# Optimization experiments

Measured on AMD Instinct MI355X. Metric: run time of the kernel, lower is better.

The kernel has to match this reference:

```python
import jax, jax.numpy as jnp
import numpy as np

FG_FRACTION = 0.5
FG_THRESH = 0.7
BG_HI = 0.5
BG_LO = 0.1
BATCHSIZE = 256
FG_ROIS = int(round(FG_FRACTION * BATCHSIZE))  # 128


def setup_inputs() -> dict:
    key = jax.random.key(0)
    k1, k2, k3 = jax.random.split(key, 3)
    N, K, C = 80000, 256, 81
    IMG = 800.0

    def make_boxes(k, n):
        ka, kb = jax.random.split(k)
        xy = jax.random.uniform(ka, (1, n, 2), dtype=jnp.float32) * (IMG - 136.0)
        wh = jax.random.uniform(kb, (1, n, 2), dtype=jnp.float32) * 128.0 + 8.0
        return jnp.concatenate([xy, xy + wh], axis=-1)  # valid x1<x2, y1<y2

    proposals = make_boxes(k1, N)          # (1, N, 4)
    gt_boxes = make_boxes(k2, K)           # (1, K, 4)
    cls = jax.random.randint(k3, (K,), 1, C)
    gt_labels = jax.nn.one_hot(cls, C, dtype=jnp.float32)[None]  # (1, K, C)
    return {"proposals": proposals, "gt_labels": gt_labels, "gt_boxes": gt_boxes}


def _iou(a, b):
    # a: (M,4), b: (K,4); keras_rcnn +1-pixel convention
    area_a = (a[:, 2] - a[:, 0] + 1.0) * (a[:, 3] - a[:, 1] + 1.0)
    area_b = (b[:, 2] - b[:, 0] + 1.0) * (b[:, 3] - b[:, 1] + 1.0)
    x1 = jnp.maximum(a[:, None, 0], b[None, :, 0])
    y1 = jnp.maximum(a[:, None, 1], b[None, :, 1])
    x2 = jnp.minimum(a[:, None, 2], b[None, :, 2])
    y2 = jnp.minimum(a[:, None, 3], b[None, :, 3])
    iw = jnp.maximum(x2 - x1 + 1.0, 0.0)
    ih = jnp.maximum(y2 - y1 + 1.0, 0.0)
    inter = iw * ih  # (M, K)
    return inter / (area_a[:, None] + area_b[None, :] - inter)


def _bbox_transform(ex, gt):
    ew = ex[:, 2] - ex[:, 0] + 1.0
    eh = ex[:, 3] - ex[:, 1] + 1.0
    ecx = ex[:, 0] + 0.5 * ew
    ecy = ex[:, 1] + 0.5 * eh
    gw = gt[:, 2] - gt[:, 0] + 1.0
    gh = gt[:, 3] - gt[:, 1] + 1.0
    gcx = gt[:, 0] + 0.5 * gw
    gcy = gt[:, 1] + 0.5 * gh
    return jnp.stack([(gcx - ecx) / ew, (gcy - ecy) / eh,
                      jnp.log(gw / ew), jnp.log(gh / eh)], axis=1)  # (B, 4)


def _forward(proposals, gt_labels, gt_boxes):
    all_rois = jnp.concatenate([proposals[0], gt_boxes[0]], axis=0)  # (M, 4)
    gt_b = gt_boxes[0]    # (K, 4)
    gt_l = gt_labels[0]   # (K, C)
    C = gt_l.shape[1]

    ov = _iou(all_rois, gt_b)               # (M, K)
    gt_assign = jnp.argmax(ov, axis=1)      # (M,)
    max_ov = jnp.max(ov, axis=1)            # (M,)

    fg_mask = max_ov >= FG_THRESH
    bg_mask = (max_ov < BG_HI) & (max_ov >= BG_LO)

    M = all_rois.shape[0]
    order = jnp.arange(M)
    # deterministic stand-in for random shuffle: candidates first, in index order
    fg_sorted = jnp.argsort(jnp.where(fg_mask, order, M + order))
    bg_sorted = jnp.argsort(jnp.where(bg_mask, order, M + order))
    num_fg = jnp.sum(fg_mask.astype(jnp.int32))
    fg_take = jnp.minimum(FG_ROIS, num_fg)

    pos = jnp.arange(BATCHSIZE)
    is_fg_slot = pos < fg_take
    keep = jnp.where(is_fg_slot,
                     fg_sorted[jnp.clip(pos, 0, M - 1)],
                     bg_sorted[jnp.clip(pos - fg_take, 0, M - 1)])  # (B,)

    rois = all_rois[keep]                    # (B, 4)
    labels = gt_l[gt_assign[keep]]           # (B, C)
    # set_label_background: bg slots -> one-hot class 0
    bg_onehot = jax.nn.one_hot(0, C, dtype=labels.dtype)
    labels = jnp.where(is_fg_slot[:, None], labels, bg_onehot[None, :])

    assigned_gt = gt_b[gt_assign[keep]]      # (B, 4)
    targets = _bbox_transform(rois, assigned_gt)  # (B, 4)

    # expand to N x 4K: only the argmax class (if > 0) gets nonzero targets
    clss = jnp.argmax(labels, axis=1)        # (B,)
    cls_oh = jnp.where((clss > 0)[:, None],
                       jax.nn.one_hot(clss, C, dtype=targets.dtype), 0.0)  # (B, C)
    bbox_targets = (cls_oh[:, :, None] * targets[:, None, :]).reshape(BATCHSIZE, 4 * C)

    return rois[None], labels[None], bbox_targets[None]


def reference(proposals, gt_labels, gt_boxes):
    return _forward(proposals, gt_labels, gt_boxes)
```

## Files before the change

kernel.cpp:

```cpp
#include <hip/hip_runtime.h>

#define FG_THRESH 0.7f
#define BG_HI 0.5f
#define BG_LO 0.1f
#define BATCH 256
#define FG_ROIS 128
#define KGT 256
#define CLS 81
#define CPT 5
#define NCHPAD 1280
#define NBIN 26
#define NSPAN 6

typedef unsigned long long ull;

__global__ __launch_bounds__(256) void k_iou(
    const float* __restrict__ proposals,
    const float* __restrict__ gt_boxes,
    int N, int M,
    int* __restrict__ gt_assign,
    ull* __restrict__ fgm,
    ull* __restrict__ bgm)
{
    __shared__ float4 gshE[KGT];
    __shared__ float garea[KGT];
    __shared__ ull pbx[4][NBIN], pby[4][NBIN];
    __shared__ ull intX[4][NBIN][NSPAN], intY[4][NBIN][NSPAN];

    int tid = threadIdx.x;
    int wv = tid >> 6, lane = tid & 63;

    float4 g = ((const float4*)gt_boxes)[tid];
    gshE[tid] = g;
    garea[tid] = (g.z - g.x + 1.0f) * (g.w - g.y + 1.0f);

    for (int b = 0; b < NBIN; ++b) {
        float hiE = 32.0f * (float)(b + 1);
        float loE = 32.0f * (float)b - 1.0f;
        ull mx = __ballot((g.x < hiE) && (g.z > loE));
        ull my = __ballot((g.y < hiE) && (g.w > loE));
        if (lane == 0) { pbx[wv][b] = mx; pby[wv][b] = my; }
    }
    __syncthreads();

    if (tid < 104) {
        int c = tid / NBIN, b = tid % NBIN;
        ull m = pbx[c][b];
        intX[c][b][0] = m;
        #pragma unroll
        for (int s = 1; s < NSPAN; ++s) {
            int bb = b + s;
            if (bb < NBIN) m |= pbx[c][bb];
            intX[c][b][s] = m;
        }
    } else if (tid >= 128 && tid < 232) {
        int u = tid - 128;
        int c = u / NBIN, b = u % NBIN;
        ull m = pby[c][b];
        intY[c][b][0] = m;
        #pragma unroll
        for (int s = 1; s < NSPAN; ++s) {
            int bb = b + s;
            if (bb < NBIN) m |= pby[c][bb];
            intY[c][b][s] = m;
        }
    }
    __syncthreads();

    int c = lane & 3;
    int rj = lane >> 2;

    int ch = blockIdx.x;
    int roi = ch * 64 + wv * 16 + rj;
    bool val = (roi < M);

    float4 a;
    if (val) a = (roi < N) ? ((const float4*)proposals)[roi] : gshE[roi - N];
    else     a = gshE[0];
    float az1 = a.z + 1.0f, aw1 = a.w + 1.0f;
    float area_a = (a.z - a.x + 1.0f) * (a.w - a.y + 1.0f);

    int b1x = (int)(a.x * 0.03125f);
    int b2x = min((int)(az1 * 0.03125f), NBIN - 1);
    int b1y = (int)(a.y * 0.03125f);
    int b2y = min((int)(aw1 * 0.03125f), NBIN - 1);
    int sx = b2x - b1x;
    int sy = b2y - b1y;

    ull mbits = val ? (intX[c][b1x][sx] & intY[c][b1y][sy]) : 0ull;

    float best = 0.0f;
    int bestk = 0;
    while (mbits) {
        int j = __ffsll(mbits) - 1;
        mbits &= mbits - 1;
        int k = (c << 6) + j;
        float4 gg = gshE[k];
        float x1 = fmaxf(a.x, gg.x);
        float y1 = fmaxf(a.y, gg.y);
        float x2 = fminf(a.z, gg.z);
        float y2 = fminf(a.w, gg.w);
        float iw = fmaxf(x2 - x1 + 1.0f, 0.0f);
        float ih = fmaxf(y2 - y1 + 1.0f, 0.0f);
        float inter = iw * ih;
        float q = inter / (area_a + garea[k] - inter);
        if (q > best) { best = q; bestk = k; }
    }

    #pragma unroll
    for (int d = 1; d < 4; d <<= 1) {
        float ob = __shfl_xor(best, d);
        int   kb = __shfl_xor(bestk, d);
        if (ob > best || (ob == best && kb < bestk)) { best = ob; bestk = kb; }
    }
    float bset = __shfl(best, (lane & 15) * 4);
    int   bk   = __shfl(bestk, (lane & 15) * 4);

    int roi2 = ch * 64 + wv * 16 + (lane & 15);
    bool isv = (lane < 16) && (roi2 < M);
    bool fgp = isv && (bset >= FG_THRESH);
    bool bgp = isv && (bset < BG_HI) && (bset >= BG_LO);
    if (isv) gt_assign[roi2] = bk;

    ull mf = __ballot(fgp);
    ull mb = __ballot(bgp);
    if (lane == 0) {
        ((unsigned short*)fgm)[(ch << 2) | wv] = (unsigned short)mf;
        ((unsigned short*)bgm)[(ch << 2) | wv] = (unsigned short)mb;
    }
}

__global__ __launch_bounds__(256) void k_finish(
    const float* __restrict__ proposals,
    const float* __restrict__ gt_boxes,
    const float* __restrict__ gt_labels,
    int N, int NCH,
    const int* __restrict__ gt_assign,
    const ull* __restrict__ fgm,
    const ull* __restrict__ bgm,
    float* __restrict__ out_rois,
    float* __restrict__ out_labels,
    float4* __restrict__ out_bbox)
{
    __shared__ ull sf[NCHPAD], sb[NCHPAD], sn[NCHPAD];
    __shared__ int pf[NCHPAD], pb[NCHPAD], pn[NCHPAD];
    __shared__ int fgl[FG_ROIS], bgl[BATCH], nbl[BATCH];
    __shared__ int wtot[3][4];
    __shared__ int lm_cls[8];
    __shared__ float4 lm_t[8];

    int tid = threadIdx.x;
    int lane = tid & 63, wv = tid >> 6;

    for (int idx = tid; idx < NCHPAD; idx += 256) {
        bool v = (idx < NCH);
        ull fv = v ? fgm[idx] : 0ull;
        ull bv = v ? bgm[idx] : 0ull;
        sf[idx] = fv;
        sb[idx] = bv;
        sn[idx] = v ? ~bv : 0ull;
    }
    __syncthreads();

    int lo = tid * CPT;
    int pc0 = 0, pc1 = 0;
    #pragma unroll
    for (int r = 0; r < CPT; ++r) {
        pc0 += __popcll(sf[lo + r]);
        pc1 += __popcll(sb[lo + r]);
    }
    int i0 = pc0, i1 = pc1;
    #pragma unroll
    for (int d = 1; d < 64; d <<= 1) {
        int t0 = __shfl_up(i0, d);
        int t1 = __shfl_up(i1, d);
        if (lane >= d) { i0 += t0; i1 += t1; }
    }
    if (lane == 63) { wtot[0][wv] = i0; wtot[1][wv] = i1; }
    __syncthreads();
    int o0 = 0, o1 = 0;
    for (int x = 0; x < wv; ++x) { o0 += wtot[0][x]; o1 += wtot[1][x]; }
    int b0 = o0 + i0 - pc0;
    int b1 = o1 + i1 - pc1;
    int num_fg = wtot[0][0] + wtot[0][1] + wtot[0][2] + wtot[0][3];
    int num_bg = wtot[1][0] + wtot[1][1] + wtot[1][2] + wtot[1][3];
    int fg_take = min(FG_ROIS, num_fg);
    bool need_nb = (fg_take + num_bg < BATCH);

    #pragma unroll
    for (int r = 0; r < CPT; ++r) {
        int w = lo + r;
        pf[w] = b0; b0 += __popcll(sf[w]);
        pb[w] = b1; b1 += __popcll(sb[w]);
    }
    __syncthreads();

    #pragma unroll
    for (int pass = 0; pass < CPT; ++pass) {
        int w = tid + 256 * pass;
        int base = pf[w];
        if (base < FG_ROIS) {
            ull m = sf[w];
            while (m) {
                if (base >= FG_ROIS) break;
                fgl[base++] = (w << 6) + __ffsll(m) - 1;
                m &= m - 1;
            }
        }
        base = pb[w];
        if (base < BATCH) {
            ull m = sb[w];
            while (m) {
                if (base >= BATCH) break;
                bgl[base++] = (w << 6) + __ffsll(m) - 1;
                m &= m - 1;
            }
        }
    }

    if (need_nb) {
        int pc2 = 0;
        #pragma unroll
        for (int r = 0; r < CPT; ++r) pc2 += __popcll(sn[lo + r]);
        int i2 = pc2;
        #pragma unroll
        for (int d = 1; d < 64; d <<= 1) {
            int t2 = __shfl_up(i2, d);
            if (lane >= d) i2 += t2;
        }
        if (lane == 63) wtot[2][wv] = i2;
        __syncthreads();
        int o2 = 0;
        for (int x = 0; x < wv; ++x) o2 += wtot[2][x];
        int b2 = o2 + i2 - pc2;
        #pragma unroll
        for (int r = 0; r < CPT; ++r) {
            int w = lo + r;
            pn[w] = b2; b2 += __popcll(sn[w]);
        }
        __syncthreads();
        #pragma unroll
        for (int pass = 0; pass < CPT; ++pass) {
            int w = tid + 256 * pass;
            int base = pn[w];
            if (base < BATCH) {
                ull m = sn[w];
                while (m) {
                    if (base >= BATCH) break;
                    nbl[base++] = (w << 6) + __ffsll(m) - 1;
                    m &= m - 1;
                }
            }
        }
    }
    __syncthreads();

    int eBase = blockIdx.x * 256;
    int posLo = eBase / CLS;
    int posHi = (eBase + 255) / CLS;
    int np = posHi - posLo + 1;

    for (int s = wv; s < np; s += 4) {
        int pos = posLo + s;
        int is_fg = (pos < fg_take) ? 1 : 0;
        int j = pos - fg_take;
        int keep = is_fg ? fgl[pos] : ((j < num_bg) ? bgl[j] : nbl[j - num_bg]);
        float4 a = (keep < N) ? ((const float4*)proposals)[keep]
                              : ((const float4*)gt_boxes)[keep - N];
        int ga = gt_assign[keep];
        float4 g = ((const float4*)gt_boxes)[ga];

        float ew = a.z - a.x + 1.0f, eh = a.w - a.y + 1.0f;
        float ecx = a.x + 0.5f * ew, ecy = a.y + 0.5f * eh;
        float gw = g.z - g.x + 1.0f, gh = g.w - g.y + 1.0f;
        float gcx = g.x + 0.5f * gw, gcy = g.y + 0.5f * gh;

        int cls = 0;
        if (is_fg) {
            float l1 = gt_labels[(size_t)ga * CLS + lane];
            int c2 = lane + 64;
            float l2 = (c2 < CLS) ? gt_labels[(size_t)ga * CLS + c2] : 0.0f;
            ull m1 = __ballot(l1 > 0.5f);
            ull m2 = __ballot(c2 < CLS && l2 > 0.5f);
            cls = m1 ? (__ffsll(m1) - 1) : (m2 ? 64 + __ffsll(m2) - 1 : 0);
        }
        if (lane == 0) {
            lm_cls[s] = cls;
            lm_t[s] = make_float4((gcx - ecx) / ew, (gcy - ecy) / eh,
                                  logf(gw / ew), logf(gh / eh));
        }
    }

    if (blockIdx.x == 0) {
        int pos = tid;
        int is_fg = (pos < fg_take) ? 1 : 0;
        int j = pos - fg_take;
        int keep = is_fg ? fgl[pos] : ((j < num_bg) ? bgl[j] : nbl[j - num_bg]);
        float4 a = (keep < N) ? ((const float4*)proposals)[keep]
                              : ((const float4*)gt_boxes)[keep - N];
        ((float4*)out_rois)[pos] = a;
    }
    __syncthreads();

    int e = eBase + tid;
    int pos = e / CLS, cc = e - pos * CLS;
    int li = pos - posLo;
    int cl = lm_cls[li];
    out_labels[e] = (cc == cl) ? 1.0f : 0.0f;
    out_bbox[e] = (cl > 0 && cc == cl) ? lm_t[li]
                                       : make_float4(0.f, 0.f, 0.f, 0.f);
}

extern "C" void kernel_launch(void* const* d_in, const int* in_sizes, int n_in,
                              void* d_out, int out_size, void* d_ws, size_t ws_size,
                              hipStream_t stream)
{
    const float* proposals = (const float*)d_in[0];
    const float* gt_labels = (const float*)d_in[1];
    const float* gt_boxes  = (const float*)d_in[2];
    int N = in_sizes[0] / 4;
    int K = in_sizes[2] / 4;
    int M = N + K;
    int NCH = (M + 63) / 64;

    char* ws = (char*)d_ws;
    size_t off = 0;
    auto alloc = [&](size_t bytes) -> void* {
        void* p = ws + off;
        off += (bytes + 255) & ~(size_t)255;
        return p;
    };
    int* gt_assign = (int*)alloc((size_t)M * 4);
    ull* fgm = (ull*)alloc((size_t)NCH * 8);
    ull* bgm = (ull*)alloc((size_t)NCH * 8);

    float* out_rois   = (float*)d_out;
    float* out_labels = out_rois + BATCH * 4;
    float4* out_bbox  = (float4*)(out_labels + BATCH * CLS);

    k_iou<<<NCH, 256, 0, stream>>>(proposals, gt_boxes, N, M,
                                   gt_assign, fgm, bgm);
    int nb2 = (BATCH * CLS) / 256;
    k_finish<<<nb2, 256, 0, stream>>>(proposals, gt_boxes, gt_labels, N, NCH,
                                      gt_assign, fgm, bgm,
                                      out_rois, out_labels, out_bbox);
    (void)K; (void)n_in; (void)out_size; (void)ws_size;
}
```

Before: 25.11 us.

## Widen finish kernel to 512 threads and compute non-bg scan unconditionally

The finish kernel now runs 512 threads per block with 3 mask words per thread, loading the masks straight into registers instead of staging them through shared memory first. The prefix scans for fg, bg and not-bg are computed together in one shuffle pass, and the separate conditional not-bg pass with its extra barriers is removed. The intent is a shorter serial scan chain and fewer block-wide syncs. In exchange every block does the not-bg scan even when it is not needed, each block handles at most 8 positions per wave, and there are half as many blocks.

```diff
diff --git a/kernel.cpp b/kernel.cpp
--- a/kernel.cpp
+++ b/kernel.cpp
@@ -7,8 +7,8 @@
 #define FG_ROIS 128
 #define KGT 256
 #define CLS 81
-#define CPT 5
-#define NCHPAD 1280
+#define NCHPAD2 1536
+#define CPT2 3
 #define NBIN 26
 #define NSPAN 6
 
@@ -69,7 +69,6 @@
 
     int c = lane & 3;
     int rj = lane >> 2;
-
     int ch = blockIdx.x;
     int roi = ch * 64 + wv * 16 + rj;
     bool val = (roi < M);
@@ -130,7 +129,7 @@
     }
 }
 
-__global__ __launch_bounds__(256) void k_finish(
+__global__ __launch_bounds__(512) void k_finish(
     const float* __restrict__ proposals,
     const float* __restrict__ gt_boxes,
     const float* __restrict__ gt_labels,
@@ -142,62 +141,70 @@
     float* __restrict__ out_labels,
     float4* __restrict__ out_bbox)
 {
-    __shared__ ull sf[NCHPAD], sb[NCHPAD], sn[NCHPAD];
-    __shared__ int pf[NCHPAD], pb[NCHPAD], pn[NCHPAD];
+    __shared__ ull sf[NCHPAD2], sb[NCHPAD2];
+    __shared__ int pf[NCHPAD2], pb[NCHPAD2], pn[NCHPAD2];
     __shared__ int fgl[FG_ROIS], bgl[BATCH], nbl[BATCH];
-    __shared__ int wtot[3][4];
+    __shared__ int wtot[3][8];
     __shared__ int lm_cls[8];
     __shared__ float4 lm_t[8];
 
     int tid = threadIdx.x;
     int lane = tid & 63, wv = tid >> 6;
-
-    for (int idx = tid; idx < NCHPAD; idx += 256) {
+    int lo = tid * CPT2;
+
+    ull wf[CPT2], wb[CPT2];
+    int vmsk[CPT2];
+    #pragma unroll
+    for (int r = 0; r < CPT2; ++r) {
+        int idx = lo + r;
         bool v = (idx < NCH);
-        ull fv = v ? fgm[idx] : 0ull;
-        ull bv = v ? bgm[idx] : 0ull;
-        sf[idx] = fv;
-        sb[idx] = bv;
-        sn[idx] = v ? ~bv : 0ull;
-    }
-    __syncthreads();
-
-    int lo = tid * CPT;
-    int pc0 = 0, pc1 = 0;
-    #pragma unroll
-    for (int r = 0; r < CPT; ++r) {
-        pc0 += __popcll(sf[lo + r]);
-        pc1 += __popcll(sb[lo + r]);
-    }
-    int i0 = pc0, i1 = pc1;
+        vmsk[r] = v;
+        wf[r] = v ? fgm[idx] : 0ull;
+        wb[r] = v ? bgm[idx] : 0ull;
+    }
+    int pc0 = 0, pc1 = 0, pc2 = 0;
+    #pragma unroll
+    for (int r = 0; r < CPT2; ++r) {
+        pc0 += __popcll(wf[r]);
+        pc1 += __popcll(wb[r]);
+        pc2 += vmsk[r] ? __popcll(~wb[r]) : 0;
+    }
+
+    int i0 = pc0, i1 = pc1, i2 = pc2;
     #pragma unroll
     for (int d = 1; d < 64; d <<= 1) {
         int t0 = __shfl_up(i0, d);
         int t1 = __shfl_up(i1, d);
-        if (lane >= d) { i0 += t0; i1 += t1; }
-    }
-    if (lane == 63) { wtot[0][wv] = i0; wtot[1][wv] = i1; }
-    __syncthreads();
-    int o0 = 0, o1 = 0;
-    for (int x = 0; x < wv; ++x) { o0 += wtot[0][x]; o1 += wtot[1][x]; }
+        int t2 = __shfl_up(i2, d);
+        if (lane >= d) { i0 += t0; i1 += t1; i2 += t2; }
+    }
+    if (lane == 63) { wtot[0][wv] = i0; wtot[1][wv] = i1; wtot[2][wv] = i2; }
+    __syncthreads();
+    int o0 = 0, o1 = 0, o2 = 0;
+    for (int x = 0; x < wv; ++x) { o0 += wtot[0][x]; o1 += wtot[1][x]; o2 += wtot[2][x]; }
     int b0 = o0 + i0 - pc0;
     int b1 = o1 + i1 - pc1;
-    int num_fg = wtot[0][0] + wtot[0][1] + wtot[0][2] + wtot[0][3];
-    int num_bg = wtot[1][0] + wtot[1][1] + wtot[1][2] + wtot[1][3];
+    int b2 = o2 + i2 - pc2;
+    int num_fg = 0, num_bg = 0;
+    #pragma unroll
+    for (int x = 0; x < 8; ++x) { num_fg += wtot[0][x]; num_bg += wtot[1][x]; }
     int fg_take = min(FG_ROIS, num_fg);
     bool need_nb = (fg_take + num_bg < BATCH);
 
     #pragma unroll
-    for (int r = 0; r < CPT; ++r) {
+    for (int r = 0; r < CPT2; ++r) {
         int w = lo + r;
-        pf[w] = b0; b0 += __popcll(sf[w]);
-        pb[w] = b1; b1 += __popcll(sb[w]);
-    }
-    __syncthreads();
-
-    #pragma unroll
-    for (int pass = 0; pass < CPT; ++pass) {
-        int w = tid + 256 * pass;
+        sf[w] = wf[r];
+        sb[w] = wb[r];
+        pf[w] = b0; b0 += __popcll(wf[r]);
+        pb[w] = b1; b1 += __popcll(wb[r]);
+        pn[w] = b2; b2 += vmsk[r] ? __popcll(~wb[r]) : 0;
+    }
+    __syncthreads();
+
+    #pragma unroll
+    for (int pass = 0; pass < CPT2; ++pass) {
+        int w = tid + 512 * pass;
         int base = pf[w];
         if (base < FG_ROIS) {
             ull m = sf[w];
@@ -216,35 +223,10 @@
                 m &= m - 1;
             }
         }
-    }
-
-    if (need_nb) {
-        int pc2 = 0;
-        #pragma unroll
-        for (int r = 0; r < CPT; ++r) pc2 += __popcll(sn[lo + r]);
-        int i2 = pc2;
-        #pragma unroll
-        for (int d = 1; d < 64; d <<= 1) {
-            int t2 = __shfl_up(i2, d);
-            if (lane >= d) i2 += t2;
-        }
-        if (lane == 63) wtot[2][wv] = i2;
-        __syncthreads();
-        int o2 = 0;
-        for (int x = 0; x < wv; ++x) o2 += wtot[2][x];
-        int b2 = o2 + i2 - pc2;
-        #pragma unroll
-        for (int r = 0; r < CPT; ++r) {
-            int w = lo + r;
-            pn[w] = b2; b2 += __popcll(sn[w]);
-        }
-        __syncthreads();
-        #pragma unroll
-        for (int pass = 0; pass < CPT; ++pass) {
-            int w = tid + 256 * pass;
-            int base = pn[w];
+        if (need_nb) {
+            base = pn[w];
             if (base < BATCH) {
-                ull m = sn[w];
+                ull m = (w < NCH) ? ~sb[w] : 0ull;
                 while (m) {
                     if (base >= BATCH) break;
                     nbl[base++] = (w << 6) + __ffsll(m) - 1;
@@ -255,13 +237,13 @@
     }
     __syncthreads();
 
-    int eBase = blockIdx.x * 256;
+    int eBase = blockIdx.x * 512;
     int posLo = eBase / CLS;
-    int posHi = (eBase + 255) / CLS;
+    int posHi = min((eBase + 511) / CLS, BATCH - 1);
     int np = posHi - posLo + 1;
 
-    for (int s = wv; s < np; s += 4) {
-        int pos = posLo + s;
+    if (wv < np) {
+        int pos = posLo + wv;
         int is_fg = (pos < fg_take) ? 1 : 0;
         int j = pos - fg_take;
         int keep = is_fg ? fgl[pos] : ((j < num_bg) ? bgl[j] : nbl[j - num_bg]);
@@ -285,13 +267,13 @@
             cls = m1 ? (__ffsll(m1) - 1) : (m2 ? 64 + __ffsll(m2) - 1 : 0);
         }
         if (lane == 0) {
-            lm_cls[s] = cls;
-            lm_t[s] = make_float4((gcx - ecx) / ew, (gcy - ecy) / eh,
-                                  logf(gw / ew), logf(gh / eh));
-        }
-    }
-
-    if (blockIdx.x == 0) {
+            lm_cls[wv] = cls;
+            lm_t[wv] = make_float4((gcx - ecx) / ew, (gcy - ecy) / eh,
+                                   logf(gw / ew), logf(gh / eh));
+        }
+    }
+
+    if (blockIdx.x == 0 && tid < BATCH) {
         int pos = tid;
         int is_fg = (pos < fg_take) ? 1 : 0;
         int j = pos - fg_take;
@@ -303,12 +285,14 @@
     __syncthreads();
 
     int e = eBase + tid;
-    int pos = e / CLS, cc = e - pos * CLS;
-    int li = pos - posLo;
-    int cl = lm_cls[li];
-    out_labels[e] = (cc == cl) ? 1.0f : 0.0f;
-    out_bbox[e] = (cl > 0 && cc == cl) ? lm_t[li]
-                                       : make_float4(0.f, 0.f, 0.f, 0.f);
+    if (e < BATCH * CLS) {
+        int pos = e / CLS, cc = e - pos * CLS;
+        int li = pos - posLo;
+        int cl = lm_cls[li];
+        out_labels[e] = (cc == cl) ? 1.0f : 0.0f;
+        out_bbox[e] = (cl > 0 && cc == cl) ? lm_t[li]
+                                           : make_float4(0.f, 0.f, 0.f, 0.f);
+    }
 }
 
 extern "C" void kernel_launch(void* const* d_in, const int* in_sizes, int n_in,
@@ -340,8 +324,8 @@
 
     k_iou<<<NCH, 256, 0, stream>>>(proposals, gt_boxes, N, M,
                                    gt_assign, fgm, bgm);
-    int nb2 = (BATCH * CLS) / 256;
-    k_finish<<<nb2, 256, 0, stream>>>(proposals, gt_boxes, gt_labels, N, NCH,
+    int nb2 = (BATCH * CLS + 511) / 512;
+    k_finish<<<nb2, 512, 0, stream>>>(proposals, gt_boxes, gt_labels, N, NCH,
                                       gt_assign, fgm, bgm,
                                       out_rois, out_labels, out_bbox);
     (void)K; (void)n_in; (void)out_size; (void)ws_size;
```

New measurement: 23.56 us. 1.07x faster.
